# Performance work log

Hardware: AMD Instinct MI355X
Metric: run time of the kernel (lower is better)

## Reference

```python
import jax, jax.numpy as jnp
import numpy as np

B, N, D_MODEL, HIDDEN, ACTION_BIN = 4096, 8, 1024, 2048, 256


def setup_inputs() -> dict:
    key = jax.random.key(0)
    k_x, k_w1, k_b1, k_w2, k_b2 = jax.random.split(key, 5)
    # per-action-dim MLP weights stacked along leading n axis
    s1 = 1.0 / np.sqrt(D_MODEL)
    s2 = 1.0 / np.sqrt(HIDDEN)
    return {
        "x": jax.random.normal(k_x, (B, N, D_MODEL), dtype=jnp.float32),
        "W1": jax.random.normal(k_w1, (N, D_MODEL, HIDDEN), dtype=jnp.float32) * s1,
        "b1": jax.random.normal(k_b1, (N, HIDDEN), dtype=jnp.float32) * s1,
        "W2": jax.random.normal(k_w2, (N, HIDDEN, ACTION_BIN), dtype=jnp.float32) * s2,
        "b2": jax.random.normal(k_b2, (N, ACTION_BIN), dtype=jnp.float32) * s2,
    }


def reference(x, W1, b1, W2, b2):
    # Original torch module loops over n slices, each with its own
    # Linear(d_model->hidden) -> ReLU -> Linear(hidden->action_bin).
    # Equivalent grouped/batched matmul over the n axis:
    x = x.astype(jnp.float32)
    h = jnp.einsum('bnd,ndh->bnh', x, W1) + b1[None, :, :]   # [b, n, hidden]
    h = jax.nn.relu(h)
    out = jnp.einsum('bnh,nha->bna', h, W2) + b2[None, :, :]  # [b, n, action_bin]
    return out
```

## Files before the change

kernel.cpp:

```cpp
#include <hip/hip_runtime.h>
#include <stdint.h>

#define BTOT   4096
#define NGRP   8
#define DMODEL 1024
#define HIDDEN 2048
#define ABIN   256

typedef short bf16x8 __attribute__((ext_vector_type(8)));
typedef float f32x4  __attribute__((ext_vector_type(4)));

__device__ __forceinline__ ushort f2bf(float f) {
    union { float f; uint32_t u; } v; v.f = f;
    return (ushort)((v.u + 0x7FFFu + ((v.u >> 16) & 1u)) >> 16);
}

__device__ __forceinline__ void gl_lds16(const ushort* g, ushort* l) {
    __builtin_amdgcn_global_load_lds(
        (const __attribute__((address_space(1))) uint32_t*)g,
        (__attribute__((address_space(3))) uint32_t*)l,
        16, 0, 0);
}

__global__ void transpose_w(const float* __restrict__ W, ushort* __restrict__ Wt,
                            int K, int N)
{
    __shared__ float tl[32][33];
    const int n  = blockIdx.y;
    const int nt = blockIdx.x % (N / 32);
    const int kt = blockIdx.x / (N / 32);
    const float* Wn  = W  + (size_t)n * K * N;
    ushort*      Wtn = Wt + (size_t)n * N * K;
    const int tx = threadIdx.x & 31, ty = threadIdx.x >> 5;
#pragma unroll
    for (int j = 0; j < 4; j++)
        tl[ty + 8 * j][tx] = Wn[(size_t)(kt * 32 + ty + 8 * j) * N + nt * 32 + tx];
    __syncthreads();
#pragma unroll
    for (int j = 0; j < 4; j++) {
        const int r = ty + 8 * j;
        Wtn[(size_t)(nt * 32 + r) * K + kt * 32 + tx] = f2bf(tl[tx][r]);
    }
}

__global__ void conv_x(const float* __restrict__ x, ushort* __restrict__ xb,
                       int CH, int cb)
{
    const int flat = blockIdx.x * 256 + threadIdx.x;
    const int d8 = flat & 127;
    const int rem = flat >> 7;
    const int n = rem & 7;
    const int r = rem >> 3;
    const float* src = x + ((size_t)(cb + r) * NGRP + n) * DMODEL + d8 * 8;
    float4 v0 = *(const float4*)(src);
    float4 v1 = *(const float4*)(src + 4);
    bf16x8 p;
    p[0] = (short)f2bf(v0.x); p[1] = (short)f2bf(v0.y);
    p[2] = (short)f2bf(v0.z); p[3] = (short)f2bf(v0.w);
    p[4] = (short)f2bf(v1.x); p[5] = (short)f2bf(v1.y);
    p[6] = (short)f2bf(v1.z); p[7] = (short)f2bf(v1.w);
    *(bf16x8*)(xb + ((size_t)n * CH + r) * DMODEL + d8 * 8) = p;
}

#define REGN(buf,op,half,ks) (sm + ((((buf)*2+(op))*2+(half))*2+(ks))*4096)

template<int MH>
__device__ __forceinline__ void mma_q(f32x4 (&acc)[8][4], const bf16x8 (&af)[4],
                                      const bf16x8 (&bv)[4])
{
#pragma unroll
    for (int m4 = 0; m4 < 4; ++m4)
#pragma unroll
        for (int nf = 0; nf < 4; ++nf)
            acc[MH * 4 + m4][nf] = __builtin_amdgcn_mfma_f32_16x16x32_bf16(
                af[m4], bv[nf], acc[MH * 4 + m4][nf], 0, 0, 0);
}

__global__ __launch_bounds__(512, 2)
void gemm8_1(const ushort* __restrict__ A, const ushort* __restrict__ Bt,
             const float* __restrict__ bias, ushort* __restrict__ h, int CH)
{
    constexpr int K = DMODEL, NDIM = HIDDEN, KT = K / 64;
    const int MT = CH >> 8, NT = NDIM >> 8;
    extern __shared__ ushort sm[];

    const int nwg = gridDim.x;
    const int bid = blockIdx.x;
    const int swz = (bid & 7) * (nwg >> 3) + (bid >> 3);
    const int n   = swz / (MT * NT);
    const int rem = swz - n * (MT * NT);
    const int mt  = rem / NT;
    const int nt  = rem - mt * NT;

    const int tid = threadIdx.x;
    const int l = tid & 63, wid = tid >> 6;
    const int wr = wid >> 2, wc = wid & 3, wc2 = wc >> 1;
    const int lq = l >> 4, lr = l & 15;

    const ushort* Ab = A  + ((size_t)n * CH   + (size_t)mt * 256) * K;
    const ushort* Bb = Bt + ((size_t)n * NDIM + (size_t)nt * 256) * K;

    const int srow = tid >> 2;
    const int sseg = (tid & 3) ^ ((tid >> 3) & 3);

    auto stageA = [&](int b, int T, int ks) {
        const size_t kofs = (size_t)T * 64 + ks * 32 + sseg * 8;
        gl_lds16(Ab + (size_t)srow * K + kofs,         REGN(b, 0, 0, ks) + tid * 8);
        gl_lds16(Ab + (size_t)(128 + srow) * K + kofs, REGN(b, 0, 1, ks) + tid * 8);
    };
    auto stageB = [&](int b, int T, int ks) {
        const size_t kofs = (size_t)T * 64 + ks * 32 + sseg * 8;
        gl_lds16(Bb + (size_t)srow * K + kofs,         REGN(b, 1, 0, ks) + tid * 8);
        gl_lds16(Bb + (size_t)(128 + srow) * K + kofs, REGN(b, 1, 1, ks) + tid * 8);
    };
    auto ldA = [&](bf16x8 (&af)[4], int b, int kk, int mh) {
#pragma unroll
        for (int m4 = 0; m4 < 4; ++m4) {
            const int rh = mh * 64 + m4 * 16 + lr;
            af[m4] = *(const bf16x8*)(REGN(b, 0, wr, kk) + rh * 32 + (lq ^ ((rh >> 1) & 3)) * 8);
        }
    };
    auto ldB = [&](bf16x8 (&bv)[4], int b, int kk) {
#pragma unroll
        for (int nf = 0; nf < 4; ++nf) {
            const int rb = (wc & 1) * 64 + nf * 16 + lr;
            bv[nf] = *(const bf16x8*)(REGN(b, 1, wc2, kk) + rb * 32 + (lq ^ ((rb >> 1) & 3)) * 8);
        }
    };

    f32x4 acc[8][4];
#pragma unroll
    for (int i = 0; i < 8; ++i)
#pragma unroll
        for (int j = 0; j < 4; ++j) acc[i][j] = (f32x4){0.f, 0.f, 0.f, 0.f};

    stageA(0, 0, 0); stageB(0, 0, 0); stageA(0, 0, 1); stageB(0, 0, 1);
    asm volatile("s_waitcnt vmcnt(4)" ::: "memory");
    __builtin_amdgcn_s_barrier();

    bf16x8 aX[4], aY[4], bv0[4], bv1[4];
    ldA(aX, 0, 0, 0); ldB(bv0, 0, 0);

    for (int g = 0; g < KT; ++g) {
        const int c = g & 1;
        const bool ns = (g + 1 < KT);

        ldA(aY, c, 0, 1);
        if (ns) stageA(c ^ 1, g + 1, 0);
        asm volatile("s_waitcnt lgkmcnt(4)" ::: "memory");
        __builtin_amdgcn_sched_barrier(0);
        __builtin_amdgcn_s_setprio(1);
        mma_q<0>(acc, aX, bv0);
        __builtin_amdgcn_s_setprio(0);
        if (ns) asm volatile("s_waitcnt vmcnt(2)" ::: "memory");
        else    asm volatile("s_waitcnt vmcnt(0)" ::: "memory");
        __builtin_amdgcn_s_barrier();

        ldA(aX, c, 1, 0); ldB(bv1, c, 1);
        if (ns) stageB(c ^ 1, g + 1, 0);
        asm volatile("s_waitcnt lgkmcnt(8)" ::: "memory");
        __builtin_amdgcn_sched_barrier(0);
        __builtin_amdgcn_s_setprio(1);
        mma_q<1>(acc, aY, bv0);
        __builtin_amdgcn_s_setprio(0);
        __builtin_amdgcn_s_barrier();

        ldA(aY, c, 1, 1);
        if (ns) stageA(c ^ 1, g + 1, 1);
        asm volatile("s_waitcnt lgkmcnt(4)" ::: "memory");
        __builtin_amdgcn_sched_barrier(0);
        __builtin_amdgcn_s_setprio(1);
        mma_q<0>(acc, aX, bv1);
        __builtin_amdgcn_s_setprio(0);
        __builtin_amdgcn_s_barrier();

        if (ns) stageB(c ^ 1, g + 1, 1);
        asm volatile("s_waitcnt lgkmcnt(0)" ::: "memory");
        __builtin_amdgcn_sched_barrier(0);
        __builtin_amdgcn_s_setprio(1);
        mma_q<1>(acc, aY, bv1);
        __builtin_amdgcn_s_setprio(0);
        if (ns) asm volatile("s_waitcnt vmcnt(4)" ::: "memory");
        __builtin_amdgcn_s_barrier();
        if (ns) { ldA(aX, c ^ 1, 0, 0); ldB(bv0, c ^ 1, 0); }
    }

    __builtin_amdgcn_sched_barrier(0);

    float bias4[4];
#pragma unroll
    for (int nf = 0; nf < 4; ++nf)
        bias4[nf] = bias[(size_t)n * NDIM + nt * 256 + wc * 64 + nf * 16 + lr];
#pragma unroll
    for (int m = 0; m < 8; ++m) {
#pragma unroll
        for (int r = 0; r < 4; ++r) {
            const int row = mt * 256 + wr * 128 + m * 16 + lq * 4 + r;
            ushort* dst = h + ((size_t)n * CH + row) * HIDDEN + nt * 256 + wc * 64 + lr;
#pragma unroll
            for (int nf = 0; nf < 4; ++nf)
                dst[nf * 16] = f2bf(fmaxf(acc[m][nf][r] + bias4[nf], 0.f));
        }
    }
}

__global__ __launch_bounds__(256, 2)
void gemm2(const ushort* __restrict__ A, const ushort* __restrict__ Bt,
           const float* __restrict__ bias, float* __restrict__ outp,
           int CH, int cb)
{
    constexpr int K = HIDDEN, NDIM = ABIN, NT = NDIM / 128, BK = 64;
    __shared__ __align__(16) ushort As[128 * BK];
    __shared__ __align__(16) ushort Bs[128 * BK];

    const int n  = blockIdx.y;
    const int mt = blockIdx.x / NT;
    const int nt = blockIdx.x % NT;

    const ushort* Ab = A  + ((size_t)n * CH   + mt * 128) * K;
    const ushort* Bb = Bt + ((size_t)n * NDIM + nt * 128) * K;

    const int t = threadIdx.x, l = t & 63, w = t >> 6;
    const int wr = w >> 1, wc = w & 1;
    const int lq = l >> 4, lr = l & 15;

    f32x4 acc[4][4];
#pragma unroll
    for (int i = 0; i < 4; i++)
#pragma unroll
        for (int j = 0; j < 4; j++) acc[i][j] = (f32x4){0.f, 0.f, 0.f, 0.f};

    for (int ki = 0; ki < K / BK; ++ki) {
        const ushort* Ak = Ab + ki * BK;
        const ushort* Bk = Bb + ki * BK;
        __syncthreads();
#pragma unroll
        for (int i = 0; i < 4; i++) {
            const int flat = t + 256 * i;
            const int row = flat >> 3;
            const int seg = (flat & 7) ^ (row & 7);
            gl_lds16(Ak + (size_t)row * K + seg * 8, (ushort*)As + flat * 8);
            gl_lds16(Bk + (size_t)row * K + seg * 8, (ushort*)Bs + flat * 8);
        }
        __syncthreads();

#pragma unroll
        for (int kk = 0; kk < 2; kk++) {
            bf16x8 af[4], bf[4];
#pragma unroll
            for (int m = 0; m < 4; m++) {
                const int row = wr * 64 + m * 16 + lr;
                af[m] = *(const bf16x8*)&As[row * BK + ((kk * 4 + lq) ^ (row & 7)) * 8];
            }
#pragma unroll
            for (int nf = 0; nf < 4; nf++) {
                const int row = wc * 64 + nf * 16 + lr;
                bf[nf] = *(const bf16x8*)&Bs[row * BK + ((kk * 4 + lq) ^ (row & 7)) * 8];
            }
#pragma unroll
            for (int m = 0; m < 4; m++)
#pragma unroll
                for (int nf = 0; nf < 4; nf++)
                    acc[m][nf] = __builtin_amdgcn_mfma_f32_16x16x32_bf16(af[m], bf[nf], acc[m][nf], 0, 0, 0);
        }
    }

#pragma unroll
    for (int nf = 0; nf < 4; nf++) {
        const int colg = nt * 128 + wc * 64 + nf * 16 + lr;
        const float bv = bias[(size_t)n * NDIM + colg];
#pragma unroll
        for (int m = 0; m < 4; m++) {
#pragma unroll
            for (int r = 0; r < 4; r++) {
                const int row = mt * 128 + wr * 64 + m * 16 + lq * 4 + r;
                outp[((size_t)(cb + row) * NGRP + n) * ABIN + colg] = acc[m][nf][r] + bv;
            }
        }
    }
}

extern "C" void kernel_launch(void* const* d_in, const int* in_sizes, int n_in,
                              void* d_out, int out_size, void* d_ws, size_t ws_size,
                              hipStream_t stream)
{
    const float* x  = (const float*)d_in[0];
    const float* W1 = (const float*)d_in[1];
    const float* b1 = (const float*)d_in[2];
    const float* W2 = (const float*)d_in[3];
    const float* b2 = (const float*)d_in[4];

    hipFuncSetAttribute((const void*)gemm8_1,
                        hipFuncAttributeMaxDynamicSharedMemorySize, 131072);

    ushort* W1t = (ushort*)d_ws;
    ushort* W2t = W1t + (size_t)NGRP * HIDDEN * DMODEL;
    ushort* xb  = W2t + (size_t)NGRP * ABIN * HIDDEN;
    const size_t fixed = ((size_t)NGRP * HIDDEN * DMODEL + (size_t)NGRP * ABIN * HIDDEN) * 2;

    int CH = 4096;
    while (CH > 256 && fixed + (size_t)CH * (NGRP * (DMODEL + HIDDEN) * 2) > ws_size) CH >>= 1;
    ushort* h = xb + (size_t)NGRP * CH * DMODEL;

    {
        dim3 g1((DMODEL / 32) * (HIDDEN / 32), NGRP);
        transpose_w<<<g1, 256, 0, stream>>>(W1, W1t, DMODEL, HIDDEN);
        dim3 g2((HIDDEN / 32) * (ABIN / 32), NGRP);
        transpose_w<<<g2, 256, 0, stream>>>(W2, W2t, HIDDEN, ABIN);
    }

    for (int cb = 0; cb < BTOT; cb += CH) {
        conv_x<<<CH * 4, 256, 0, stream>>>(x, xb, CH, cb);
        const int g1 = NGRP * (CH / 256) * (HIDDEN / 256);
        gemm8_1<<<g1, 512, 131072, stream>>>(xb, W1t, b1, h, CH);
        dim3 g2((CH / 128) * (ABIN / 128), NGRP);
        gemm2<<<g2, 256, 0, stream>>>(h, W2t, b2, (float*)d_out, CH, cb);
    }
}
```

Baseline: 257.5 us.

## Restructure GEMM main loop with deeper LDS fragment prefetch and paired staging

Rewrites the software pipeline of the first GEMM's K-loop. It uses six register fragment buffers instead of four, so LDS-to-register loads for the next sub-step are issued further ahead of the MFMAs that consume them. Global-to-LDS staging of A and B halves is now issued in pairs, with full vmcnt(0) waits at the phase boundaries. The aim is to hide LDS latency better, at the cost of more VGPR pressure and coarser global-load waits.

New measurement: 259.5 us. Within noise of the previous version (+0.8%).

```diff
diff --git a/kernel.cpp b/kernel.cpp
--- a/kernel.cpp
+++ b/kernel.cpp
@@ -134,55 +134,62 @@
 #pragma unroll
         for (int j = 0; j < 4; ++j) acc[i][j] = (f32x4){0.f, 0.f, 0.f, 0.f};
 
-    stageA(0, 0, 0); stageB(0, 0, 0); stageA(0, 0, 1); stageB(0, 0, 1);
-    asm volatile("s_waitcnt vmcnt(4)" ::: "memory");
+    stageA(0, 0, 0); stageB(0, 0, 0);
+    stageA(0, 0, 1); stageB(0, 0, 1);
+    asm volatile("s_waitcnt vmcnt(0)" ::: "memory");
     __builtin_amdgcn_s_barrier();
 
-    bf16x8 aX[4], aY[4], bv0[4], bv1[4];
-    ldA(aX, 0, 0, 0); ldB(bv0, 0, 0);
+    bf16x8 a0[4], a1[4], a2[4], a3[4], bE[4], bO[4];
+    ldA(a0, 0, 0, 0); ldB(bE, 0, 0);
+    ldA(a1, 0, 0, 1);
 
     for (int g = 0; g < KT; ++g) {
         const int c = g & 1;
         const bool ns = (g + 1 < KT);
 
-        ldA(aY, c, 0, 1);
-        if (ns) stageA(c ^ 1, g + 1, 0);
-        asm volatile("s_waitcnt lgkmcnt(4)" ::: "memory");
+        if (ns) { stageA(c ^ 1, g + 1, 0); stageB(c ^ 1, g + 1, 0); }
+        ldA(a2, c, 1, 0); ldB(bO, c, 1);
+        asm volatile("s_waitcnt lgkmcnt(12)" ::: "memory");
         __builtin_amdgcn_sched_barrier(0);
         __builtin_amdgcn_s_setprio(1);
-        mma_q<0>(acc, aX, bv0);
+        mma_q<0>(acc, a0, bE);
         __builtin_amdgcn_s_setprio(0);
-        if (ns) asm volatile("s_waitcnt vmcnt(2)" ::: "memory");
-        else    asm volatile("s_waitcnt vmcnt(0)" ::: "memory");
         __builtin_amdgcn_s_barrier();
 
-        ldA(aX, c, 1, 0); ldB(bv1, c, 1);
-        if (ns) stageB(c ^ 1, g + 1, 0);
-        asm volatile("s_waitcnt lgkmcnt(8)" ::: "memory");
+        ldA(a3, c, 1, 1);
+        asm volatile("s_waitcnt lgkmcnt(12)" ::: "memory");
         __builtin_amdgcn_sched_barrier(0);
         __builtin_amdgcn_s_setprio(1);
-        mma_q<1>(acc, aY, bv0);
+        mma_q<1>(acc, a1, bE);
+        __builtin_amdgcn_s_setprio(0);
+        if (ns) asm volatile("s_waitcnt vmcnt(0)" ::: "memory");
+        __builtin_amdgcn_s_barrier();
+
+        if (ns) {
+            stageA(c ^ 1, g + 1, 1); stageB(c ^ 1, g + 1, 1);
+            ldA(a0, c ^ 1, 0, 0); ldB(bE, c ^ 1, 0);
+            asm volatile("s_waitcnt lgkmcnt(12)" ::: "memory");
+        } else {
+            asm volatile("s_waitcnt lgkmcnt(4)" ::: "memory");
+        }
+        __builtin_amdgcn_sched_barrier(0);
+        __builtin_amdgcn_s_setprio(1);
+        mma_q<0>(acc, a2, bO);
         __builtin_amdgcn_s_setprio(0);
         __builtin_amdgcn_s_barrier();
 
-        ldA(aY, c, 1, 1);
-        if (ns) stageA(c ^ 1, g + 1, 1);
-        asm volatile("s_waitcnt lgkmcnt(4)" ::: "memory");
+        if (ns) {
+            ldA(a1, c ^ 1, 0, 1);
+            asm volatile("s_waitcnt lgkmcnt(12)" ::: "memory");
+        } else {
+            asm volatile("s_waitcnt lgkmcnt(0)" ::: "memory");
+        }
         __builtin_amdgcn_sched_barrier(0);
         __builtin_amdgcn_s_setprio(1);
-        mma_q<0>(acc, aX, bv1);
+        mma_q<1>(acc, a3, bO);
         __builtin_amdgcn_s_setprio(0);
+        if (ns) asm volatile("s_waitcnt vmcnt(0)" ::: "memory");
         __builtin_amdgcn_s_barrier();
-
-        if (ns) stageB(c ^ 1, g + 1, 1);
-        asm volatile("s_waitcnt lgkmcnt(0)" ::: "memory");
-        __builtin_amdgcn_sched_barrier(0);
-        __builtin_amdgcn_s_setprio(1);
-        mma_q<1>(acc, aY, bv1);
-        __builtin_amdgcn_s_setprio(0);
-        if (ns) asm volatile("s_waitcnt vmcnt(4)" ::: "memory");
-        __builtin_amdgcn_s_barrier();
-        if (ns) { ldA(aX, c ^ 1, 0, 0); ldB(bv0, c ^ 1, 0); }
     }
 
     __builtin_amdgcn_sched_barrier(0);
```
